# Kernel optimization log

Hardware: AMD Instinct MI355X
Metric: run time of the kernel (lower is better)

The kernel has to match this reference:

```python
import jax, jax.numpy as jnp
import numpy as np

B, N, C, NS = 4, 2048, 128, 64
RADIUS = 0.25
BN_EPS = 1e-5


def _ball_query(xyz):
    """First-NS point indices within RADIUS of each point (pointnet2 semantics:
    indices taken in ascending point order, short balls padded with the first hit).
    xyz: (B,N,3) -> idx: (B,N,NS) int32."""
    sq = jnp.sum(xyz * xyz, axis=-1)                                   # (B,N)
    d2 = sq[:, :, None] + sq[:, None, :] - 2.0 * jnp.einsum('bnd,bmd->bnm', xyz, xyz)
    within = d2 < RADIUS ** 2                                          # (B,N,N)
    cand = jnp.where(within, jnp.arange(N, dtype=jnp.int32)[None, None, :], N)
    idx = jnp.sort(cand, axis=-1)[..., :NS]                            # first NS hits
    idx = jnp.where(idx == N, idx[..., :1], idx)                       # pad with first hit
    return idx


def _bn_relu(h, g, b):
    # eval-mode BatchNorm2d with running_mean=0, running_var=1, then ReLU
    inv = 1.0 / jnp.sqrt(1.0 + BN_EPS)
    return jax.nn.relu(g[None, :, None, None] * (h * inv) + b[None, :, None, None])


def _forward(xyz, features, W1, W2, W3, g1, g2, g3, b1, b2, b3):
    idx = _ball_query(xyz)                                             # (B,N,NS)
    bidx = jnp.arange(B)[:, None, None]
    g_xyz = xyz[bidx, idx]                                             # (B,N,NS,3)
    grouped_xyz = jnp.transpose(g_xyz - xyz[:, :, None, :], (0, 3, 1, 2))  # (B,3,N,NS) relative
    feat_t = jnp.transpose(features, (0, 2, 1))                        # (B,N,C)
    g_feat = jnp.transpose(feat_t[bidx, idx], (0, 3, 1, 2))            # (B,C,N,NS)
    grouped_features = jnp.concatenate([grouped_xyz, g_feat], axis=1)  # (B,3+C,N,NS)

    xyz_feature = jnp.concatenate([jnp.transpose(xyz, (0, 2, 1)), features], axis=1)  # (B,3+C,N)
    center = jax.lax.stop_gradient(xyz_feature)[..., None]             # .detach() in torch
    diff = grouped_features - center
    h = diff * diff                                                    # squared diff

    h = _bn_relu(jnp.einsum('oc,bcns->bons', W1, h), g1, b1)           # (B,256,N,NS)
    h = _bn_relu(jnp.einsum('oc,bcns->bons', W2, h), g2, b2)           # (B,128,N,NS)
    h = _bn_relu(jnp.einsum('oc,bcns->bons', W3, h), g3, b3)           # (B,1,N,NS)

    shift = jnp.sum(grouped_xyz * h, axis=-1)                          # (B,3,N)
    return shift / jnp.sum(h, axis=-1)                                 # / (B,1,N)


def setup_inputs() -> dict:
    key = jax.random.key(0)
    ks = jax.random.split(key, 5)
    cin = C + 3
    return {
        'xyz': jax.random.uniform(ks[0], (B, N, 3), dtype=jnp.float32),
        'features': jax.random.normal(ks[1], (B, C, N), dtype=jnp.float32),
        'W1': jax.random.normal(ks[2], (256, cin), dtype=jnp.float32) * np.float32(np.sqrt(2.0 / cin)),
        'W2': jax.random.normal(ks[3], (128, 256), dtype=jnp.float32) * np.float32(np.sqrt(2.0 / 256)),
        'W3': jax.random.normal(ks[4], (1, 128), dtype=jnp.float32) * np.float32(np.sqrt(2.0 / 128)),
        'g1': jnp.ones((256,), jnp.float32), 'g2': jnp.ones((128,), jnp.float32), 'g3': jnp.ones((1,), jnp.float32),
        'b1': jnp.zeros((256,), jnp.float32), 'b2': jnp.zeros((128,), jnp.float32), 'b3': jnp.zeros((1,), jnp.float32),
    }


def reference(xyz, features, W1, W2, W3, g1, g2, g3, b1, b2, b3):
    return _forward(xyz, features, W1, W2, W3, g1, g2, g3, b1, b2, b3)
```

## Files before the change

### kernel.cpp

```cpp
#include <hip/hip_runtime.h>
#include <math.h>

typedef _Float16 f16;
typedef _Float16 f16x8 __attribute__((ext_vector_type(8)));
typedef float f32x4 __attribute__((ext_vector_type(4)));

#define B_  4
#define N_  2048
#define C_  128
#define NS_ 64

#define WS_FEAT16 0u
#define WS_IDX    2097152u
#define WS_W1P    3145728u
#define WS_W2P    3211264u

#define OFF_H   0
#define OFF_W   16384
#define OFF_A2  0
#define OFF_GX  33792
#define OFF_QF  34560
#define OFF_IDX 35072
#define OFF_RED 35072
#define OFF_W3  35328
#define LDS_TOTAL 35840

__device__ __forceinline__ void gl_lds16(const char* gp, char* lp) {
  __builtin_amdgcn_global_load_lds(
      (const __attribute__((address_space(1))) unsigned int*)gp,
      (__attribute__((address_space(3))) unsigned int*)lp, 16, 0, 0);
}

__device__ __forceinline__ unsigned pk2(float a, float b) {
  union { f16 h[2]; unsigned u; } cv;
  cv.h[0] = (f16)a; cv.h[1] = (f16)b;
  return cv.u;
}

__global__ __launch_bounds__(256) void prep_kernel(
    const float* __restrict__ feat, const float* __restrict__ W1,
    const float* __restrict__ W2, f16* __restrict__ feat16,
    char* __restrict__ W1p, char* __restrict__ W2p)
{
  int i = blockIdx.x * 256 + threadIdx.x;
  {
    int n = i & (N_ - 1);
    int bc = i >> 11;
    int c = bc & (C_ - 1);
    int b = bc >> 7;
    feat16[(size_t)((b << 11) + n) * C_ + c] = (f16)feat[i];
  }
  if (i < 8 * 2048) {
    int sl = i >> 11; int r = i & 2047; int op = r >> 4; int j = r & 15;
    int g = sl >> 1, oh = sl & 1;
    int o = oh * 128 + op;
    const float* row = W1 + o * 131 + 3 + g * 32 + 2 * j;
    unsigned byte = ((unsigned)(op * 64 + j * 4)) ^ ((unsigned)(((op >> 1) & 7) << 4));
    *(unsigned*)(W1p + (size_t)sl * 8192 + byte) = pk2(row[0], row[1]);
  }
  if (i < 8 * 2048) {
    int ko = i >> 11; int r = i & 2047; int p = r >> 4; int j = r & 15;
    int o = ko * 32 + 2 * j;
    unsigned byte = ((unsigned)(p * 64 + j * 4)) ^ ((unsigned)(((p >> 1) & 7) << 4));
    *(unsigned*)(W2p + (size_t)ko * 8192 + byte) = pk2(W2[p * 256 + o], W2[p * 256 + o + 1]);
  }
}

__global__ __launch_bounds__(256) void ballquery_kernel(
    const float* __restrict__ xyz, unsigned short* __restrict__ idxout)
{
  __shared__ float  xl[N_ * 3];
  __shared__ double sq[N_];
  __shared__ int    ibuf[4][NS_];

  const int b  = blockIdx.x >> 9;
  const int ng = blockIdx.x & 511;
  const int t  = threadIdx.x;
  const float* xb = xyz + (size_t)b * N_ * 3;

  for (int i = t; i < N_ * 3; i += 256) xl[i] = xb[i];
  __syncthreads();
  for (int i = t; i < N_; i += 256) {
    double x = (double)xl[3*i], y = (double)xl[3*i+1], z = (double)xl[3*i+2];
    sq[i] = x*x + y*y + z*z;
  }
  __syncthreads();

  const int wv = t >> 6, lane = t & 63;
  const int n = ng * 4 + wv;
  const double xn = (double)xl[3*n], yn = (double)xl[3*n+1], zn = (double)xl[3*n+2];
  const double sn = sq[n];

  int cnt = 0;
  for (int mb = 0; mb < N_; mb += 64) {
    int m = mb + lane;
    double dot = xn*(double)xl[3*m] + yn*(double)xl[3*m+1] + zn*(double)xl[3*m+2];
    double d2 = (sn + sq[m]) - 2.0 * dot;
    bool hit = d2 < 0.0625;
    unsigned long long mask = __ballot(hit);
    int pos = __popcll(mask & ((1ULL << lane) - 1ULL));
    int slot = cnt + pos;
    if (hit && slot < NS_) ibuf[wv][slot] = m;
    cnt += (int)__popcll(mask);
    if (cnt >= NS_) break;
  }
  asm volatile("s_waitcnt lgkmcnt(0)" ::: "memory");
  int total = cnt < NS_ ? cnt : NS_;
  int v = ibuf[wv][lane < total ? lane : 0];
  idxout[((size_t)b * N_ + n) * NS_ + lane] = (unsigned short)v;
}

__global__ __launch_bounds__(256, 3) void mlp_kernel(
    const float* __restrict__ xyz, const f16* __restrict__ feat16,
    const char* __restrict__ w1p, const char* __restrict__ w2p,
    const unsigned short* __restrict__ idxg,
    const float* __restrict__ W1g, const float* __restrict__ W3g,
    const float* __restrict__ g1, const float* __restrict__ b1,
    const float* __restrict__ g2, const float* __restrict__ b2,
    const float* __restrict__ g3, const float* __restrict__ b3,
    float* __restrict__ out)
{
  __shared__ __attribute__((aligned(128))) char lds[LDS_TOTAL];

  const int bidRaw = blockIdx.x;
  const int bn = ((bidRaw & 7) << 10) + (bidRaw >> 3);
  const int b = bn >> 11;
  const int n = bn & (N_ - 1);
  const int t = threadIdx.x;
  const int w = t >> 6, lane = t & 63;
  const int l15 = lane & 15, lg = lane >> 4;
  const unsigned labase = ((unsigned)(l15 * 64 + lg * 16)) ^ ((unsigned)(((l15 >> 1) & 7) << 4));
  const float inv = 1.0f / sqrtf(1.0f + 1e-5f);

  float gg1v[4], bo1v[4];
  float wx[4][3];
  #pragma unroll
  for (int nt = 0; nt < 4; ++nt) {
    int o = (nt >> 1) * 128 + 32 * w + (nt & 1) * 16 + l15;
    gg1v[nt] = g1[o] * inv; bo1v[nt] = b1[o];
    #pragma unroll
    for (int c = 0; c < 3; ++c) wx[nt][c] = W1g[o * 131 + c];
  }
  float gg2v[2], bo2v[2];
  #pragma unroll
  for (int nt = 0; nt < 2; ++nt) {
    int p = 32 * w + nt * 16 + l15;
    gg2v[nt] = g2[p] * inv; bo2v[nt] = b2[p];
  }
  const float g3c = g3[0] * inv, b3c = b3[0];
  const float xn0 = xyz[(size_t)bn*3+0], xn1 = xyz[(size_t)bn*3+1], xn2 = xyz[(size_t)bn*3+2];

  auto STAGE = [&](int sl) {
    const char* gp = (sl < 8 ? w1p + (size_t)sl * 8192
                             : w2p + (size_t)(sl - 8) * 8192) + t * 16;
    char* lp = lds + OFF_W + ((sl & 1) << 13) + (w << 10);
    gl_lds16(gp, lp);
    gl_lds16(gp + 4096, lp + 4096);
  };

  f32x4 acc1[4][4];
  f32x4 acc2[4][2] = {};

  STAGE(0);
  if (t < 64) ((int*)(lds + OFF_IDX))[t] = (int)idxg[(size_t)bn * 64 + t];
  if (t < 64) ((unsigned*)(lds + OFF_QF))[t] =
      ((const unsigned*)(feat16 + (size_t)bn * C_))[t];
  if (t < 128) ((float*)(lds + OFF_W3))[t] = W3g[t];
  __syncthreads();

  const int* idxl = (const int*)(lds + OFF_IDX);

  {
    int s = t & 63, g = t >> 6;
    int m = idxl[s];
    const f16* pb = feat16 + ((size_t)b * N_ + m) * C_ + g * 32;
    const f16* qb = (const f16*)(lds + OFF_QF) + g * 32;
    const unsigned sw = ((unsigned)((s >> 1) & 7)) << 4;
    const unsigned base = (unsigned)(g * 4096) ;
    #pragma unroll
    for (int qq = 0; qq < 4; ++qq) {
      f16x8 p = *(const f16x8*)(pb + qq * 8);
      f16x8 q = *(const f16x8*)(qb + qq * 8);
      f16x8 d = p - q;
      f16x8 hh = d * d;
      unsigned byte = base
        + ((((unsigned)(s * 64 + qq * 16)) ^ sw ^ ((unsigned)((g & 3) << 4))));
      *(f16x8*)(lds + OFF_H + byte) = hh;
    }
  }
  if (t < 192) {
    int s = t & 63, c = t >> 6;
    int m = idxl[s];
    float p = xyz[((size_t)b * N_ + m) * 3 + c];
    float xnc = (c == 0) ? xn0 : (c == 1 ? xn1 : xn2);
    ((float*)(lds + OFF_GX))[s * 3 + c] = p - xnc;
  }
  asm volatile("s_waitcnt vmcnt(0)" ::: "memory");
  __syncthreads();

  {
    const float* gx = (const float*)(lds + OFF_GX);
    #pragma unroll
    for (int mt = 0; mt < 4; ++mt)
      #pragma unroll
      for (int r = 0; r < 4; ++r) {
        int s = mt * 16 + lg * 4 + r;
        float d0 = gx[s * 3 + 0] - xn0;
        float d1 = gx[s * 3 + 1] - xn1;
        float d2 = gx[s * 3 + 2] - xn2;
        d0 *= d0; d1 *= d1; d2 *= d2;
        #pragma unroll
        for (int nt = 0; nt < 4; ++nt)
          acc1[mt][nt][r] = fmaf(wx[nt][0], d0, fmaf(wx[nt][1], d1, wx[nt][2] * d2));
      }
  }

  f16x8 af[4];
  #pragma unroll
  for (int p = 0; p < 8; ++p) {
    const int g = p >> 1, oh = p & 1;
    STAGE(p + 1);
    if (oh == 0) {
      const char* hb = lds + OFF_H + g * 4096;
      const unsigned gx4 = ((unsigned)(g & 3)) << 4;
      #pragma unroll
      for (int mt = 0; mt < 4; ++mt)
        af[mt] = *(const f16x8*)(hb + mt * 1024 + (labase ^ gx4));
    }
    const char* wb = lds + OFF_W + ((p & 1) << 13);
    f16x8 bf0 = *(const f16x8*)(wb + (32 * w) * 64 + labase);
    f16x8 bf1 = *(const f16x8*)(wb + (32 * w + 16) * 64 + labase);
    __builtin_amdgcn_s_setprio(1);
    #pragma unroll
    for (int mt = 0; mt < 4; ++mt) {
      acc1[mt][oh * 2 + 0] =
          __builtin_amdgcn_mfma_f32_16x16x32_f16(af[mt], bf0, acc1[mt][oh * 2 + 0], 0, 0, 0);
      acc1[mt][oh * 2 + 1] =
          __builtin_amdgcn_mfma_f32_16x16x32_f16(af[mt], bf1, acc1[mt][oh * 2 + 1], 0, 0, 0);
    }
    __builtin_amdgcn_s_setprio(0);
    asm volatile("s_waitcnt vmcnt(0)" ::: "memory");
    __syncthreads();
  }

  auto EPI1 = [&](int hf) {
    #pragma unroll
    for (int mt = 0; mt < 4; ++mt)
      #pragma unroll
      for (int nt2 = 0; nt2 < 2; ++nt2) {
        const int nt = hf * 2 + nt2;
        #pragma unroll
        for (int r = 0; r < 4; ++r) {
          int s = mt * 16 + lg * 4 + r;
          float a = fmaf(acc1[mt][nt][r], gg1v[nt], bo1v[nt]);
          a = a > 0.0f ? a : 0.0f;
          unsigned byte = (unsigned)(w * 4096)
            + (((unsigned)(s * 64 + nt2 * 32 + l15 * 2)) ^ ((unsigned)(((s >> 1) & 7) << 4))
               ^ ((unsigned)((w & 3) << 4)));
          *(f16*)(lds + OFF_H + byte) = (f16)a;
        }
      }
  };
  EPI1(0);
  __syncthreads();

  #pragma unroll
  for (int ko = 0; ko < 8; ++ko) {
    if (ko < 7) STAGE(9 + ko);
    const char* ab = lds + OFF_H + (ko & 3) * 4096;
    const unsigned gx4 = ((unsigned)(ko & 3)) << 4;
    f16x8 a2f[4];
    #pragma unroll
    for (int mt = 0; mt < 4; ++mt)
      a2f[mt] = *(const f16x8*)(ab + mt * 1024 + (labase ^ gx4));
    const char* wb = lds + OFF_W + ((ko & 1) << 13);
    f16x8 bf0 = *(const f16x8*)(wb + (32 * w) * 64 + labase);
    f16x8 bf1 = *(const f16x8*)(wb + (32 * w + 16) * 64 + labase);
    __builtin_amdgcn_s_setprio(1);
    #pragma unroll
    for (int mt = 0; mt < 4; ++mt) {
      acc2[mt][0] =
          __builtin_amdgcn_mfma_f32_16x16x32_f16(a2f[mt], bf0, acc2[mt][0], 0, 0, 0);
      acc2[mt][1] =
          __builtin_amdgcn_mfma_f32_16x16x32_f16(a2f[mt], bf1, acc2[mt][1], 0, 0, 0);
    }
    __builtin_amdgcn_s_setprio(0);
    asm volatile("s_waitcnt vmcnt(0)" ::: "memory");
    __syncthreads();
    if (ko == 3) {
      EPI1(1);
      __syncthreads();
    }
  }

  #pragma unroll
  for (int mt = 0; mt < 4; ++mt)
    #pragma unroll
    for (int nt2 = 0; nt2 < 2; ++nt2) {
      int p2 = 32 * w + nt2 * 16 + l15;
      #pragma unroll
      for (int r = 0; r < 4; ++r) {
        int s = mt * 16 + lg * 4 + r;
        float a = fmaf(acc2[mt][nt2][r], gg2v[nt2], bo2v[nt2]);
        a = a > 0.0f ? a : 0.0f;
        *(float*)(lds + OFF_A2 + s * 528 + p2 * 4) = a;
      }
    }
  __syncthreads();

  {
    int s3 = t >> 2, q3 = t & 3;
    const float* a2row = (const float*)(lds + OFF_A2) + s3 * 132;
    const float* w3r = (const float*)(lds + OFF_W3);
    float z3 = 0.0f;
    #pragma unroll
    for (int i = 0; i < 8; ++i) {
      f32x4 av = *(const f32x4*)(a2row + q3 * 32 + i * 4);
      f32x4 wv = *(const f32x4*)(w3r + q3 * 32 + i * 4);
      z3 = fmaf(av[0], wv[0], z3); z3 = fmaf(av[1], wv[1], z3);
      z3 = fmaf(av[2], wv[2], z3); z3 = fmaf(av[3], wv[3], z3);
    }
    z3 += __shfl_xor(z3, 1);
    z3 += __shfl_xor(z3, 2);
    float wgt = fmaf(g3c, z3, b3c);
    wgt = wgt > 0.0f ? wgt : 0.0f;
    float v0 = 0.f, v1 = 0.f, v2 = 0.f, v3 = 0.f;
    if (q3 == 0) {
      const float* gx = (const float*)(lds + OFF_GX) + s3 * 3;
      v0 = gx[0] * wgt; v1 = gx[1] * wgt; v2 = gx[2] * wgt; v3 = wgt;
    }
    #pragma unroll
    for (int off = 4; off < 64; off <<= 1) {
      v0 += __shfl_xor(v0, off); v1 += __shfl_xor(v1, off);
      v2 += __shfl_xor(v2, off); v3 += __shfl_xor(v3, off);
    }
    if (lane == 0) {
      float* red = (float*)(lds + OFF_RED);
      red[w * 4 + 0] = v0; red[w * 4 + 1] = v1;
      red[w * 4 + 2] = v2; red[w * 4 + 3] = v3;
    }
    __syncthreads();
    if (t == 0) {
      const float* red = (const float*)(lds + OFF_RED);
      float n0 = red[0] + red[4] + red[8]  + red[12];
      float n1 = red[1] + red[5] + red[9]  + red[13];
      float n2 = red[2] + red[6] + red[10] + red[14];
      float dd = red[3] + red[7] + red[11] + red[15];
      out[(size_t)(b * 3 + 0) * N_ + n] = n0 / dd;
      out[(size_t)(b * 3 + 1) * N_ + n] = n1 / dd;
      out[(size_t)(b * 3 + 2) * N_ + n] = n2 / dd;
    }
  }
}

extern "C" void kernel_launch(void* const* d_in, const int* in_sizes, int n_in,
                              void* d_out, int out_size, void* d_ws, size_t ws_size,
                              hipStream_t stream) {
  (void)in_sizes; (void)n_in; (void)out_size; (void)ws_size;
  const float* xyz      = (const float*)d_in[0];
  const float* features = (const float*)d_in[1];
  const float* W1 = (const float*)d_in[2];
  const float* W2 = (const float*)d_in[3];
  const float* W3 = (const float*)d_in[4];
  const float* g1 = (const float*)d_in[5];
  const float* g2 = (const float*)d_in[6];
  const float* g3 = (const float*)d_in[7];
  const float* b1 = (const float*)d_in[8];
  const float* b2 = (const float*)d_in[9];
  const float* b3 = (const float*)d_in[10];
  float* out = (float*)d_out;

  char* ws = (char*)d_ws;
  f16* feat16         = (f16*)(ws + WS_FEAT16);
  unsigned short* idx = (unsigned short*)(ws + WS_IDX);
  char* W1p           = ws + WS_W1P;
  char* W2p           = ws + WS_W2P;

  prep_kernel<<<dim3((B_ * C_ * N_) / 256), dim3(256), 0, stream>>>(
      features, W1, W2, feat16, W1p, W2p);
  ballquery_kernel<<<dim3(B_ * N_ / 4), dim3(256), 0, stream>>>(xyz, idx);
  mlp_kernel<<<dim3(B_ * N_), dim3(256), 0, stream>>>(
      xyz, feat16, W1p, W2p, idx, W1, W3, g1, b1, g2, b2, g3, b3, out);
}
```

Before: 141.4 us.

## Move xyz term of layer 1 to MFMA and widen weight staging slices

The three xyz channels of layer 1 now go through a small 16x16x16 MFMA against a padded W1x slice in LDS, replacing per-thread scalar FMAs and the per-thread W1 register loads. Weight slices are doubled to 16KB so the layer-1 and layer-2 loops each run 4 iterations instead of 8. The full __syncthreads with vmcnt(0) drain is replaced by partial vmcnt waits plus raw s_barrier, so the next slice's loads can stay in flight while the current one is consumed. This raises LDS use from about 35KB to 53KB per block, which may limit occupancy, and adds extra barriers per iteration.

```diff
diff --git a/kernel.cpp b/kernel.cpp
--- a/kernel.cpp
+++ b/kernel.cpp
@@ -3,6 +3,7 @@
 
 typedef _Float16 f16;
 typedef _Float16 f16x8 __attribute__((ext_vector_type(8)));
+typedef _Float16 f16x4 __attribute__((ext_vector_type(4)));
 typedef float f32x4 __attribute__((ext_vector_type(4)));
 
 #define B_  4
@@ -12,18 +13,20 @@
 
 #define WS_FEAT16 0u
 #define WS_IDX    2097152u
-#define WS_W1P    3145728u
-#define WS_W2P    3211264u
+#define WS_W1X    3145728u
+#define WS_W1P    3153920u
+#define WS_W2P    3219456u
 
 #define OFF_H   0
-#define OFF_W   16384
+#define OFF_HX  16384
+#define OFF_W   18432
 #define OFF_A2  0
-#define OFF_GX  33792
-#define OFF_QF  34560
-#define OFF_IDX 35072
-#define OFF_RED 35072
-#define OFF_W3  35328
-#define LDS_TOTAL 35840
+#define OFF_GX  51200
+#define OFF_QF  51968
+#define OFF_IDX 52480
+#define OFF_RED 52480
+#define OFF_W3  52736
+#define LDS_TOTAL 53248
 
 __device__ __forceinline__ void gl_lds16(const char* gp, char* lp) {
   __builtin_amdgcn_global_load_lds(
@@ -40,7 +43,7 @@
 __global__ __launch_bounds__(256) void prep_kernel(
     const float* __restrict__ feat, const float* __restrict__ W1,
     const float* __restrict__ W2, f16* __restrict__ feat16,
-    char* __restrict__ W1p, char* __restrict__ W2p)
+    char* __restrict__ W1x, char* __restrict__ W1p, char* __restrict__ W2p)
 {
   int i = blockIdx.x * 256 + threadIdx.x;
   {
@@ -50,19 +53,24 @@
     int b = bc >> 7;
     feat16[(size_t)((b << 11) + n) * C_ + c] = (f16)feat[i];
   }
-  if (i < 8 * 2048) {
-    int sl = i >> 11; int r = i & 2047; int op = r >> 4; int j = r & 15;
-    int g = sl >> 1, oh = sl & 1;
-    int o = oh * 128 + op;
+  if (i < 16384) {
+    int g = i >> 12, r = i & 4095, o = r >> 4, j = r & 15;
     const float* row = W1 + o * 131 + 3 + g * 32 + 2 * j;
-    unsigned byte = ((unsigned)(op * 64 + j * 4)) ^ ((unsigned)(((op >> 1) & 7) << 4));
-    *(unsigned*)(W1p + (size_t)sl * 8192 + byte) = pk2(row[0], row[1]);
-  }
-  if (i < 8 * 2048) {
-    int ko = i >> 11; int r = i & 2047; int p = r >> 4; int j = r & 15;
-    int o = ko * 32 + 2 * j;
-    unsigned byte = ((unsigned)(p * 64 + j * 4)) ^ ((unsigned)(((p >> 1) & 7) << 4));
-    *(unsigned*)(W2p + (size_t)ko * 8192 + byte) = pk2(W2[p * 256 + o], W2[p * 256 + o + 1]);
+    unsigned byte = ((unsigned)(o * 64 + j * 4)) ^ ((unsigned)(((o >> 1) & 7) << 4));
+    *(unsigned*)(W1p + (size_t)g * 16384 + byte) = pk2(row[0], row[1]);
+  }
+  if (i < 16384) {
+    int ko = i >> 12, r = i & 4095, p = r >> 5, j = r & 31;
+    int o = ko * 64 + 2 * j;
+    unsigned byte = ((unsigned)(p * 128 + j * 4)) ^ ((unsigned)(((p >> 1) & 7) << 4));
+    *(unsigned*)(W2p + (size_t)ko * 16384 + byte) = pk2(W2[p * 256 + o], W2[p * 256 + o + 1]);
+  }
+  if (i < 2048) {
+    int o = i >> 3, j = i & 7;
+    unsigned v = 0;
+    if (j == 0)      v = pk2(W1[o * 131 + 0], W1[o * 131 + 1]);
+    else if (j == 1) v = pk2(W1[o * 131 + 2], 0.0f);
+    *(unsigned*)(W1x + o * 32 + j * 4) = v;
   }
 }
 
@@ -112,9 +120,10 @@
 
 __global__ __launch_bounds__(256, 3) void mlp_kernel(
     const float* __restrict__ xyz, const f16* __restrict__ feat16,
-    const char* __restrict__ w1p, const char* __restrict__ w2p,
+    const char* __restrict__ w1x, const char* __restrict__ w1p,
+    const char* __restrict__ w2p,
     const unsigned short* __restrict__ idxg,
-    const float* __restrict__ W1g, const float* __restrict__ W3g,
+    const float* __restrict__ W3g,
     const float* __restrict__ g1, const float* __restrict__ b1,
     const float* __restrict__ g2, const float* __restrict__ b2,
     const float* __restrict__ g3, const float* __restrict__ b3,
@@ -129,17 +138,17 @@
   const int t = threadIdx.x;
   const int w = t >> 6, lane = t & 63;
   const int l15 = lane & 15, lg = lane >> 4;
-  const unsigned labase = ((unsigned)(l15 * 64 + lg * 16)) ^ ((unsigned)(((l15 >> 1) & 7) << 4));
+  const unsigned swzl = (unsigned)(((l15 >> 1) & 7) << 4);
+  const unsigned labase = ((unsigned)(l15 * 64 + lg * 16)) ^ swzl;
+  const unsigned w2b0 = ((unsigned)(l15 * 128 + lg * 16)) ^ swzl;
+  const unsigned w2b1 = ((unsigned)(l15 * 128 + 64 + lg * 16)) ^ swzl;
   const float inv = 1.0f / sqrtf(1.0f + 1e-5f);
 
   float gg1v[4], bo1v[4];
-  float wx[4][3];
   #pragma unroll
   for (int nt = 0; nt < 4; ++nt) {
     int o = (nt >> 1) * 128 + 32 * w + (nt & 1) * 16 + l15;
     gg1v[nt] = g1[o] * inv; bo1v[nt] = b1[o];
-    #pragma unroll
-    for (int c = 0; c < 3; ++c) wx[nt][c] = W1g[o * 131 + c];
   }
   float gg2v[2], bo2v[2];
   #pragma unroll
@@ -151,11 +160,14 @@
   const float xn0 = xyz[(size_t)bn*3+0], xn1 = xyz[(size_t)bn*3+1], xn2 = xyz[(size_t)bn*3+2];
 
   auto STAGE = [&](int sl) {
-    const char* gp = (sl < 8 ? w1p + (size_t)sl * 8192
-                             : w2p + (size_t)(sl - 8) * 8192) + t * 16;
-    char* lp = lds + OFF_W + ((sl & 1) << 13) + (w << 10);
-    gl_lds16(gp, lp);
-    gl_lds16(gp + 4096, lp + 4096);
+    const char* gp; int nloads;
+    if (sl == 0)      { gp = w1x;                          nloads = 2; }
+    else if (sl <= 4) { gp = w1p + (size_t)(sl - 1) * 16384; nloads = 4; }
+    else              { gp = w2p + (size_t)(sl - 5) * 16384; nloads = 4; }
+    gp += t * 16;
+    char* lp = lds + OFF_W + ((sl & 1) << 14) + (w << 10);
+    for (int i = 0; i < nloads; ++i)
+      gl_lds16(gp + i * 4096, lp + i * 4096);
   };
 
   f32x4 acc1[4][4];
@@ -176,7 +188,7 @@
     const f16* pb = feat16 + ((size_t)b * N_ + m) * C_ + g * 32;
     const f16* qb = (const f16*)(lds + OFF_QF) + g * 32;
     const unsigned sw = ((unsigned)((s >> 1) & 7)) << 4;
-    const unsigned base = (unsigned)(g * 4096) ;
+    const unsigned base = (unsigned)(g * 4096);
     #pragma unroll
     for (int qq = 0; qq < 4; ++qq) {
       f16x8 p = *(const f16x8*)(pb + qq * 8);
@@ -188,59 +200,78 @@
       *(f16x8*)(lds + OFF_H + byte) = hh;
     }
   }
-  if (t < 192) {
-    int s = t & 63, c = t >> 6;
+  if (t < 64) {
+    int s = t;
     int m = idxl[s];
-    float p = xyz[((size_t)b * N_ + m) * 3 + c];
-    float xnc = (c == 0) ? xn0 : (c == 1 ? xn1 : xn2);
-    ((float*)(lds + OFF_GX))[s * 3 + c] = p - xnc;
-  }
-  asm volatile("s_waitcnt vmcnt(0)" ::: "memory");
-  __syncthreads();
-
+    const float* pm = xyz + ((size_t)b * N_ + m) * 3;
+    float p0 = pm[0], p1 = pm[1], p2c = pm[2];
+    float* gxp = (float*)(lds + OFF_GX) + s * 3;
+    gxp[0] = p0 - xn0; gxp[1] = p1 - xn1; gxp[2] = p2c - xn2;
+    float h0 = p0 - 2.0f * xn0; h0 *= h0;
+    float h1 = p1 - 2.0f * xn1; h1 *= h1;
+    float h2 = p2c - 2.0f * xn2; h2 *= h2;
+    char* hx = lds + OFF_HX + s * 32;
+    *(unsigned*)(hx + 0)  = pk2(h0, h1);
+    *(unsigned*)(hx + 4)  = pk2(h2, 0.0f);
+    *(unsigned*)(hx + 8)  = 0u;
+    *(unsigned*)(hx + 12) = 0u;
+    f32x4 z4 = {0.0f, 0.0f, 0.0f, 0.0f};
+    *(f32x4*)(hx + 16) = z4;
+  }
+
+  STAGE(1);
+  asm volatile("s_waitcnt vmcnt(4) lgkmcnt(0)" ::: "memory");
+  __builtin_amdgcn_s_barrier();
   {
-    const float* gx = (const float*)(lds + OFF_GX);
+    const char* wbx = lds + OFF_W;
+    f16x4 bf4[4];
+    #pragma unroll
+    for (int nt = 0; nt < 4; ++nt) {
+      int orow = (nt >> 1) * 128 + 32 * w + (nt & 1) * 16 + l15;
+      bf4[nt] = *(const f16x4*)(wbx + orow * 32 + lg * 8);
+    }
+    asm volatile("s_waitcnt lgkmcnt(0)" ::: "memory");
+    __builtin_amdgcn_s_barrier();
+    f16x4 af4[4];
+    #pragma unroll
+    for (int mt = 0; mt < 4; ++mt)
+      af4[mt] = *(const f16x4*)(lds + OFF_HX + (16 * mt + l15) * 32 + lg * 8);
+    const f32x4 z4 = {0.0f, 0.0f, 0.0f, 0.0f};
     #pragma unroll
     for (int mt = 0; mt < 4; ++mt)
       #pragma unroll
-      for (int r = 0; r < 4; ++r) {
-        int s = mt * 16 + lg * 4 + r;
-        float d0 = gx[s * 3 + 0] - xn0;
-        float d1 = gx[s * 3 + 1] - xn1;
-        float d2 = gx[s * 3 + 2] - xn2;
-        d0 *= d0; d1 *= d1; d2 *= d2;
-        #pragma unroll
-        for (int nt = 0; nt < 4; ++nt)
-          acc1[mt][nt][r] = fmaf(wx[nt][0], d0, fmaf(wx[nt][1], d1, wx[nt][2] * d2));
-      }
-  }
-
-  f16x8 af[4];
+      for (int nt = 0; nt < 4; ++nt)
+        acc1[mt][nt] = __builtin_amdgcn_mfma_f32_16x16x16f16(af4[mt], bf4[nt], z4, 0, 0, 0);
+  }
+
   #pragma unroll
-  for (int p = 0; p < 8; ++p) {
-    const int g = p >> 1, oh = p & 1;
-    STAGE(p + 1);
-    if (oh == 0) {
-      const char* hb = lds + OFF_H + g * 4096;
-      const unsigned gx4 = ((unsigned)(g & 3)) << 4;
+  for (int g = 0; g < 4; ++g) {
+    const int sl = 1 + g;
+    STAGE(sl + 1);
+    asm volatile("s_waitcnt vmcnt(4) lgkmcnt(0)" ::: "memory");
+    __builtin_amdgcn_s_barrier();
+    const char* wb = lds + OFF_W + ((sl & 1) << 14);
+    f16x8 bf[4];
+    #pragma unroll
+    for (int nt = 0; nt < 4; ++nt) {
+      int ob = (nt >> 1) * 128 + 32 * w + (nt & 1) * 16;
+      bf[nt] = *(const f16x8*)(wb + ob * 64 + labase);
+    }
+    asm volatile("s_waitcnt lgkmcnt(0)" ::: "memory");
+    __builtin_amdgcn_s_barrier();
+    const char* hb = lds + OFF_H + g * 4096;
+    const unsigned gx4 = ((unsigned)g) << 4;
+    f16x8 af[4];
+    #pragma unroll
+    for (int mt = 0; mt < 4; ++mt)
+      af[mt] = *(const f16x8*)(hb + mt * 1024 + (labase ^ gx4));
+    __builtin_amdgcn_s_setprio(1);
+    #pragma unroll
+    for (int mt = 0; mt < 4; ++mt)
       #pragma unroll
-      for (int mt = 0; mt < 4; ++mt)
-        af[mt] = *(const f16x8*)(hb + mt * 1024 + (labase ^ gx4));
-    }
-    const char* wb = lds + OFF_W + ((p & 1) << 13);
-    f16x8 bf0 = *(const f16x8*)(wb + (32 * w) * 64 + labase);
-    f16x8 bf1 = *(const f16x8*)(wb + (32 * w + 16) * 64 + labase);
-    __builtin_amdgcn_s_setprio(1);
-    #pragma unroll
-    for (int mt = 0; mt < 4; ++mt) {
-      acc1[mt][oh * 2 + 0] =
-          __builtin_amdgcn_mfma_f32_16x16x32_f16(af[mt], bf0, acc1[mt][oh * 2 + 0], 0, 0, 0);
-      acc1[mt][oh * 2 + 1] =
-          __builtin_amdgcn_mfma_f32_16x16x32_f16(af[mt], bf1, acc1[mt][oh * 2 + 1], 0, 0, 0);
-    }
+      for (int nt = 0; nt < 4; ++nt)
+        acc1[mt][nt] = __builtin_amdgcn_mfma_f32_16x16x32_f16(af[mt], bf[nt], acc1[mt][nt], 0, 0, 0);
     __builtin_amdgcn_s_setprio(0);
-    asm volatile("s_waitcnt vmcnt(0)" ::: "memory");
-    __syncthreads();
   }
 
   auto EPI1 = [&](int hf) {
@@ -261,37 +292,60 @@
         }
       }
   };
+  asm volatile("s_waitcnt lgkmcnt(0)" ::: "memory");
+  __builtin_amdgcn_s_barrier();
   EPI1(0);
-  __syncthreads();
+  asm volatile("s_waitcnt lgkmcnt(0)" ::: "memory");
+  __builtin_amdgcn_s_barrier();
 
   #pragma unroll
-  for (int ko = 0; ko < 8; ++ko) {
-    if (ko < 7) STAGE(9 + ko);
-    const char* ab = lds + OFF_H + (ko & 3) * 4096;
-    const unsigned gx4 = ((unsigned)(ko & 3)) << 4;
-    f16x8 a2f[4];
-    #pragma unroll
-    for (int mt = 0; mt < 4; ++mt)
-      a2f[mt] = *(const f16x8*)(ab + mt * 1024 + (labase ^ gx4));
-    const char* wb = lds + OFF_W + ((ko & 1) << 13);
-    f16x8 bf0 = *(const f16x8*)(wb + (32 * w) * 64 + labase);
-    f16x8 bf1 = *(const f16x8*)(wb + (32 * w + 16) * 64 + labase);
+  for (int k = 0; k < 4; ++k) {
+    const int sl = 5 + k;
+    if (sl < 8) {
+      STAGE(sl + 1);
+      asm volatile("s_waitcnt vmcnt(4) lgkmcnt(0)" ::: "memory");
+    } else {
+      asm volatile("s_waitcnt vmcnt(0) lgkmcnt(0)" ::: "memory");
+    }
+    __builtin_amdgcn_s_barrier();
+    const char* wb = lds + OFF_W + ((sl & 1) << 14);
+    f16x8 bq0[2], bq1[2];
+    #pragma unroll
+    for (int nt2 = 0; nt2 < 2; ++nt2) {
+      int pb = (32 * w + nt2 * 16) * 128;
+      bq0[nt2] = *(const f16x8*)(wb + pb + w2b0);
+      bq1[nt2] = *(const f16x8*)(wb + pb + w2b1);
+    }
+    asm volatile("s_waitcnt lgkmcnt(0)" ::: "memory");
+    __builtin_amdgcn_s_barrier();
+    const int sl0 = (2 * k) & 3, sl1 = (2 * k + 1) & 3;
+    f16x8 a0f[4], a1f[4];
+    #pragma unroll
+    for (int mt = 0; mt < 4; ++mt) {
+      a0f[mt] = *(const f16x8*)(lds + OFF_H + sl0 * 4096 + mt * 1024 + (labase ^ (unsigned)(sl0 << 4)));
+      a1f[mt] = *(const f16x8*)(lds + OFF_H + sl1 * 4096 + mt * 1024 + (labase ^ (unsigned)(sl1 << 4)));
+    }
     __builtin_amdgcn_s_setprio(1);
     #pragma unroll
-    for (int mt = 0; mt < 4; ++mt) {
-      acc2[mt][0] =
-          __builtin_amdgcn_mfma_f32_16x16x32_f16(a2f[mt], bf0, acc2[mt][0], 0, 0, 0);
-      acc2[mt][1] =
-          __builtin_amdgcn_mfma_f32_16x16x32_f16(a2f[mt], bf1, acc2[mt][1], 0, 0, 0);
-    }
+    for (int mt = 0; mt < 4; ++mt)
+      #pragma unroll
+      for (int nt2 = 0; nt2 < 2; ++nt2) {
+        f32x4 c = acc2[mt][nt2];
+        c = __builtin_amdgcn_mfma_f32_16x16x32_f16(a0f[mt], bq0[nt2], c, 0, 0, 0);
+        c = __builtin_amdgcn_mfma_f32_16x16x32_f16(a1f[mt], bq1[nt2], c, 0, 0, 0);
+        acc2[mt][nt2] = c;
+      }
     __builtin_amdgcn_s_setprio(0);
-    asm volatile("s_waitcnt vmcnt(0)" ::: "memory");
-    __syncthreads();
-    if (ko == 3) {
+    if (k == 1) {
+      asm volatile("s_waitcnt lgkmcnt(0)" ::: "memory");
+      __builtin_amdgcn_s_barrier();
       EPI1(1);
-      __syncthreads();
-    }
-  }
+      asm volatile("s_waitcnt lgkmcnt(0)" ::: "memory");
+      __builtin_amdgcn_s_barrier();
+    }
+  }
+  asm volatile("s_waitcnt lgkmcnt(0)" ::: "memory");
+  __builtin_amdgcn_s_barrier();
 
   #pragma unroll
   for (int mt = 0; mt < 4; ++mt)
@@ -306,7 +360,8 @@
         *(float*)(lds + OFF_A2 + s * 528 + p2 * 4) = a;
       }
     }
-  __syncthreads();
+  asm volatile("s_waitcnt lgkmcnt(0)" ::: "memory");
+  __builtin_amdgcn_s_barrier();
 
   {
     int s3 = t >> 2, q3 = t & 3;
@@ -373,12 +428,13 @@
   char* ws = (char*)d_ws;
   f16* feat16         = (f16*)(ws + WS_FEAT16);
   unsigned short* idx = (unsigned short*)(ws + WS_IDX);
+  char* W1x           = ws + WS_W1X;
   char* W1p           = ws + WS_W1P;
   char* W2p           = ws + WS_W2P;
 
   prep_kernel<<<dim3((B_ * C_ * N_) / 256), dim3(256), 0, stream>>>(
-      features, W1, W2, feat16, W1p, W2p);
+      features, W1, W2, feat16, W1x, W1p, W2p);
   ballquery_kernel<<<dim3(B_ * N_ / 4), dim3(256), 0, stream>>>(xyz, idx);
   mlp_kernel<<<dim3(B_ * N_), dim3(256), 0, stream>>>(
-      xyz, feat16, W1p, W2p, idx, W1, W3, g1, b1, g2, b2, g3, b3, out);
-}
+      xyz, feat16, W1x, W1p, W2p, idx, W3, g1, b1, g2, b2, g3, b3, out);
+}
```

After: 136.2 us. 3.7% less time.
